# Kernel tuning notes

Hardware: AMD Instinct MI355X
Metric: run time of the kernel (lower is better)

## Reference

```python
import jax, jax.numpy as jnp
import numpy as np

CHUNK = 128
KERNEL_EPS = 1e-4
ATTN_EPS = 1e-6


def _gaussian_orthogonal_random_matrix(nb_rows, nb_cols, seed=0):
    # scaling=0: rows of stacked orthogonal blocks, scaled by chi-distributed norms
    rng = np.random.default_rng(seed)
    blocks = []
    n_full = nb_rows // nb_cols
    for _ in range(n_full):
        qm, _ = np.linalg.qr(rng.standard_normal((nb_cols, nb_cols)))
        blocks.append(qm.T)
    rem = nb_rows - n_full * nb_cols
    if rem > 0:
        qm, _ = np.linalg.qr(rng.standard_normal((nb_cols, nb_cols)))
        blocks.append(qm.T[:rem])
    mat = np.concatenate(blocks, axis=0)
    multiplier = np.linalg.norm(rng.standard_normal((nb_rows, nb_cols)), axis=1)
    return (multiplier[:, None] * mat).astype(np.float32)


def softmax_kernel(data, proj, is_query):
    # data: [b,h,n,d], proj: [m,d]
    d = data.shape[-1]
    m = proj.shape[0]
    data_normalizer = d ** -0.25
    ratio = m ** -0.5
    data_dash = jnp.einsum('bhnd,md->bhnm', data * data_normalizer, proj)
    diag_data = (data ** 2).sum(-1, keepdims=True) * 0.5 * (data_normalizer ** 2)
    if is_query:
        stab = jnp.max(data_dash, axis=-1, keepdims=True)
    else:
        stab = jnp.max(data_dash)
    return ratio * (jnp.exp(data_dash - diag_data - stab) + KERNEL_EPS)


def chunked_causal_linear_attention(qf, kf, v):
    # qf,kf: [b,h,n,m]; v: [b,h,n,e]
    b, h, n, m = qf.shape
    e = v.shape[-1]
    nc = n // CHUNK
    to_chunks = lambda t: t.reshape(b, h, nc, CHUNK, -1).transpose(2, 0, 1, 3, 4)
    qc, kc, vc = to_chunks(qf), to_chunks(kf), to_chunks(v)  # [nc,b,h,c,*]

    def step(carry, xs):
        Z, S = carry  # Z: [b,h,m], S: [b,h,m,e]
        q, k, vv = xs
        k_cum = Z[:, :, None, :] + jnp.cumsum(k, axis=2)          # [b,h,c,m]
        D_inv = 1.0 / jnp.einsum('bhcm,bhcm->bhc', q, k_cum + ATTN_EPS)
        ctx = jnp.einsum('bhcm,bhce->bhcme', k, vv)               # [b,h,c,m,e]
        ctx_cum = S[:, :, None, :, :] + jnp.cumsum(ctx, axis=2)
        out = jnp.einsum('bhcme,bhcm,bhc->bhce', ctx_cum, q, D_inv)
        return (k_cum[:, :, -1, :], ctx_cum[:, :, -1, :, :]), out

    Z0 = jnp.zeros((b, h, m), qf.dtype)
    S0 = jnp.zeros((b, h, m, e), qf.dtype)
    (Z, S), outs = jax.lax.scan(jax.checkpoint(step), (Z0, S0), (qc, kc, vc))
    out = outs.transpose(1, 2, 0, 3, 4).reshape(b, h, n, e)
    return out, Z, S


def setup_inputs() -> dict:
    key = jax.random.key(0)
    kq, kk, kv = jax.random.split(key, 3)
    B, H, N, D, M = 2, 8, 4096, 64, 256
    q = jax.random.normal(kq, (B, H, N, D), dtype=jnp.float32)
    k = jax.random.normal(kk, (B, H, N, D), dtype=jnp.float32)
    v = jax.random.normal(kv, (B, H, N, D), dtype=jnp.float32)
    projection_matrix = jnp.asarray(_gaussian_orthogonal_random_matrix(M, D))
    return {"q": q, "k": k, "v": v, "projection_matrix": projection_matrix,
            "inferrring_states": 1}


def reference(q, k, v, projection_matrix, inferrring_states):
    qf = softmax_kernel(q, projection_matrix, is_query=True)
    kf = softmax_kernel(k, projection_matrix, is_query=False)
    out, Z, S = chunked_causal_linear_attention(qf, kf, v)
    return (out, Z, S)
```

## Files before the change

kernel.cpp:

```cpp
#include <hip/hip_runtime.h>

typedef unsigned short ushort_t;
typedef __attribute__((ext_vector_type(8))) short bf16x8;
typedef __attribute__((ext_vector_type(8))) _Float16 f16x8;
typedef __attribute__((ext_vector_type(16))) float f32x16;

#define NORMC 0.35355339059327373f
#define DIAGC 0.0625f
#define RATIO 0.0625f
#define KEPS  1e-4f
#define AEPS  1e-6f
#define KAPPA (RATIO*KEPS)

__device__ __forceinline__ unsigned short f2bf(float f){
  unsigned u = __float_as_uint(f);
  unsigned r = (u + 0x7FFFu + ((u >> 16) & 1u)) >> 16;
  return (unsigned short)r;
}
__device__ __forceinline__ float bf2f(unsigned short h){
  return __uint_as_float(((unsigned)h) << 16);
}
__device__ __forceinline__ unsigned enc_f(float f){
  unsigned u = __float_as_uint(f);
  return (u & 0x80000000u) ? ~u : (u | 0x80000000u);
}
__device__ __forceinline__ float dec_f(unsigned e){
  unsigned b = (e & 0x80000000u) ? (e ^ 0x80000000u) : ~e;
  return __uint_as_float(b);
}
__device__ __forceinline__ unsigned short h2u(_Float16 h){
  union { _Float16 h; unsigned short u; } c; c.h = h; return c.u;
}
__device__ __forceinline__ unsigned pk2h(float a, float b){
  return (unsigned)h2u((_Float16)a) | ((unsigned)h2u((_Float16)b) << 16);
}
__device__ __forceinline__ unsigned cvt2(unsigned wrd, float alpha){
  float lo = bf2f((ushort_t)(wrd & 0xffffu));
  float hi = bf2f((ushort_t)(wrd >> 16));
  return (unsigned)f2bf(fmaf(alpha, lo, KAPPA)) |
         ((unsigned)f2bf(fmaf(alpha, hi, KAPPA)) << 16);
}

__global__ void k_prep(const float* __restrict__ proj, ushort_t* __restrict__ pjh,
                       unsigned* __restrict__ kmax){
  int t = threadIdx.x;
  if (t == 0) *kmax = 0u;
  for (int d = 0; d < 64; ++d){
    float val = NORMC * proj[t*64 + d];
    pjh[t*64 + d] = h2u((_Float16)val);
  }
}

__launch_bounds__(512, 4)
__global__ void k_feat(const float* __restrict__ q, const float* __restrict__ k,
                       const ushort_t* __restrict__ pjh,
                       ushort_t* __restrict__ qf, ushort_t* __restrict__ kfp,
                       unsigned* __restrict__ kmax, float* __restrict__ lmArr)
{
  extern __shared__ char sm[];
  char* Bp = sm;
  char* Xh = sm + 32768;
  char* Xl = sm + 49152;
  float* dsm  = (float*)(sm + 65536);
  float* rmx  = (float*)(sm + 66048);
  float* wred = (float*)(sm + 67072);

  int tid = threadIdx.x;
  int w   = tid >> 6;
  int wr  = w & 3;
  int wc  = w >> 2;
  int lane= tid & 63;
  int l31 = lane & 31;
  int half= lane >> 5;

  bool isQ = (blockIdx.x < 512);
  int tile = isQ ? (int)blockIdx.x : (int)blockIdx.x - 512;
  const float* src = isQ ? q : k;
  int row0 = tile * 128;

  for (int i = tid; i < 2048; i += 512){
    int m = i >> 3, c8 = i & 7;
    int rgn = ((m>>5)*4 + (c8>>1))*2 + (c8&1);
    int slot = (m & 31) ^ ((rgn & 7) << 2);
    *(uint4*)(Bp + rgn*512 + slot*16) = *(const uint4*)(pjh + m*64 + c8*8);
  }
  #pragma unroll
  for (int it = 0; it < 4; ++it){
    int g = it*512 + tid;
    int row = g >> 4, c4 = g & 15;
    float4 xv = *(const float4*)(src + (size_t)(row0+row)*64 + c4*4);
    _Float16 h0=(_Float16)xv.x, h1=(_Float16)xv.y, h2=(_Float16)xv.z, h3=(_Float16)xv.w;
    float l0 = xv.x-(float)h0, l1 = xv.y-(float)h1, l2 = xv.z-(float)h2, l3 = xv.w-(float)h3;
    int rgn = ((row>>5)*4 + (c4>>2))*2 + ((c4>>1)&1);
    int off = rgn*512 + (((row&31) ^ ((c4>>1)<<2)))*16 + (c4&1)*8;
    uint2 ph; ph.x = (unsigned)h2u(h0)|((unsigned)h2u(h1)<<16);
              ph.y = (unsigned)h2u(h2)|((unsigned)h2u(h3)<<16);
    uint2 pl; pl.x = pk2h(l0,l1); pl.y = pk2h(l2,l3);
    *(uint2*)(Xh + off) = ph;
    *(uint2*)(Xl + off) = pl;
    float ssq = xv.x*xv.x + xv.y*xv.y + xv.z*xv.z + xv.w*xv.w;
    ssq += __shfl_xor(ssq, 1); ssq += __shfl_xor(ssq, 2);
    ssq += __shfl_xor(ssq, 4); ssq += __shfl_xor(ssq, 8);
    if ((tid & 15) == 0) dsm[row] = ssq;
  }
  __syncthreads();

  f16x8 ah[4], al[4];
  #pragma unroll
  for (int ks = 0; ks < 4; ++ks){
    int rgn = (wr*4+ks)*2+half;
    int off = rgn*512 + ((l31 ^ ((2*ks+half)<<2)))*16;
    ah[ks] = *(const f16x8*)(Xh + off);
    al[ks] = *(const f16x8*)(Xl + off);
  }
  f32x16 acc[4];
  #pragma unroll
  for (int ct=0; ct<4; ++ct){
    #pragma unroll
    for (int r=0; r<16; ++r) acc[ct][r] = 0.f;
  }
  #pragma unroll
  for (int ks = 0; ks < 4; ++ks){
    #pragma unroll
    for (int ct=0; ct<4; ++ct){
      int ctg = wc*4 + ct;
      int rgn = (ctg*4+ks)*2+half;
      f16x8 bv = *(const f16x8*)(Bp + rgn*512 + ((l31 ^ ((2*ks+half)<<2)))*16);
      acc[ct] = __builtin_amdgcn_mfma_f32_32x32x16_f16(ah[ks], bv, acc[ct], 0, 0, 0);
      acc[ct] = __builtin_amdgcn_mfma_f32_32x32x16_f16(al[ks], bv, acc[ct], 0, 0, 0);
    }
  }

  float rmax[16];
  #pragma unroll
  for (int r=0; r<16; ++r){
    float mx = acc[0][r];
    #pragma unroll
    for (int ct=1; ct<4; ++ct) mx = fmaxf(mx, acc[ct][r]);
    #pragma unroll
    for (int s=1; s<32; s<<=1) mx = fmaxf(mx, __shfl_xor(mx, s));
    rmax[r] = mx;
  }
  if (isQ){
    if (l31 == 0){
      #pragma unroll
      for (int r=0; r<16; ++r)
        rmx[wc*128 + 32*wr + (r&3) + 8*(r>>2) + 4*half] = rmax[r];
    }
  } else {
    float wm = rmax[0];
    #pragma unroll
    for (int r=1; r<16; ++r) wm = fmaxf(wm, rmax[r]);
    wm = fmaxf(wm, __shfl_xor(wm, 32));
    if (lane == 0) wred[w] = wm;
  }
  __syncthreads();

  float lmb = 0.f;
  if (!isQ){
    lmb = wred[0];
    #pragma unroll
    for (int i=1;i<8;++i) lmb = fmaxf(lmb, wred[i]);
    if (tid == 0){
      lmArr[tile] = lmb;
      atomicMax(kmax, enc_f(lmb));
    }
  }
  float dgv[16], stv[16];
  #pragma unroll
  for (int r=0; r<16; ++r){
    int lrow = 32*wr + (r&3) + 8*(r>>2) + 4*half;
    dgv[r] = DIAGC * dsm[lrow];
    stv[r] = isQ ? fmaxf(rmx[lrow], rmx[128+lrow]) : lmb;
  }

  char* ob = sm;
  #pragma unroll
  for (int r=0; r<16; ++r){
    int lrow = 32*wr + (r&3) + 8*(r>>2) + 4*half;
    #pragma unroll
    for (int ct=0; ct<4; ++ct){
      int col = wc*128 + ct*32 + l31;
      float e = __expf(acc[ct][r] - dgv[r] - stv[r]);
      float val = isQ ? RATIO*(e + KEPS) : e;
      *(ushort_t*)(ob + lrow*512 + ((col*2) ^ ((lrow&15)<<4))) = f2bf(val);
    }
  }
  __syncthreads();
  ushort_t* dst = (isQ ? qf : kfp) + (size_t)row0*256;
  for (int i = tid; i < 4096; i += 512){
    int row = i >> 5, s = i & 31;
    uint4 d = *(const uint4*)(ob + row*512 + ((s*16) ^ ((row&15)<<4)));
    *(uint4*)(dst + (size_t)row*256 + ((s ^ (row&15)))*8) = d;
  }
}

__launch_bounds__(256)
__global__ void k_chunk(const ushort_t* __restrict__ kfp, const float* __restrict__ v,
                        float* __restrict__ Zl, float* __restrict__ Sl,
                        const float* __restrict__ lmArr, const unsigned* __restrict__ kmax){
  extern __shared__ char sm[];
  char* kT = sm;
  char* vT = sm + 65536;
  int tid = threadIdx.x;
  int w   = tid >> 6;
  int lane= tid & 63;
  int l31 = lane & 31;
  int half= lane >> 5;
  int bh = blockIdx.x >> 5, j = blockIdx.x & 31;
  int row0 = bh*4096 + j*128;
  int cb = bh*32 + j;

  float gmv = dec_f(*kmax);
  float alpha = RATIO * __expf(lmArr[cb] - gmv);

  {
    const ushort_t* kp = kfp + (size_t)row0*256 + tid;
    char* krow = kT + tid*256;
    int swz = (tid & 15) << 4;
    #pragma unroll 16
    for (int c=0; c<128; ++c){
      float val = fmaf(alpha, bf2f(kp[(size_t)c*256]), KAPPA);
      *(ushort_t*)(krow + ((c*2) ^ swz)) = f2bf(val);
    }
  }
  {
    int e = tid & 63; int c0 = tid >> 6;
    char* vrow = vT + e*256;
    int swz = (e & 15) << 4;
    #pragma unroll 8
    for (int u=0; u<32; ++u){
      int c = c0 + u*4;
      float vv = v[(size_t)(row0+c)*64 + e];
      *(ushort_t*)(vrow + ((c*2) ^ swz)) = f2bf(vv);
    }
  }
  __syncthreads();

  f32x16 acc[2][2];
  f32x16 accz[2];
  #pragma unroll
  for (int a=0;a<2;++a){
    #pragma unroll
    for (int b=0;b<2;++b){
      #pragma unroll
      for (int r=0;r<16;++r) acc[a][b][r]=0.f;
    }
    #pragma unroll
    for (int r=0;r<16;++r) accz[a][r]=0.f;
  }
  bf16x8 onesf;
  #pragma unroll
  for (int i=0;i<8;++i) onesf[i] = (l31==0) ? (short)0x3F80 : (short)0;

  #pragma unroll
  for (int ks=0; ks<8; ++ks){
    int koff = ks*32 + half*16;
    bf16x8 af[2], bf[2];
    #pragma unroll
    for (int mt=0; mt<2; ++mt){
      int m = (2*w + mt)*32 + l31;
      af[mt] = *(const bf16x8*)(kT + m*256 + (koff ^ ((m&15)<<4)));
    }
    #pragma unroll
    for (int et=0; et<2; ++et){
      int e = et*32 + l31;
      bf[et] = *(const bf16x8*)(vT + e*256 + (koff ^ ((e&15)<<4)));
    }
    #pragma unroll
    for (int mt=0; mt<2; ++mt){
      accz[mt] = __builtin_amdgcn_mfma_f32_32x32x16_bf16(af[mt], onesf, accz[mt], 0, 0, 0);
      #pragma unroll
      for (int et=0; et<2; ++et)
        acc[mt][et] = __builtin_amdgcn_mfma_f32_32x32x16_bf16(af[mt], bf[et], acc[mt][et], 0, 0, 0);
    }
  }

  #pragma unroll
  for (int mt=0; mt<2; ++mt){
    #pragma unroll
    for (int r=0; r<16; ++r){
      int m = (2*w + mt)*32 + (r&3) + 8*(r>>2) + 4*half;
      #pragma unroll
      for (int et=0; et<2; ++et){
        int e = et*32 + l31;
        Sl[(size_t)cb*16384 + (size_t)m*64 + e] = acc[mt][et][r];
      }
    }
  }
  if (l31 == 0){
    #pragma unroll
    for (int mt=0; mt<2; ++mt){
      #pragma unroll
      for (int r=0; r<16; ++r){
        int m = (2*w + mt)*32 + (r&3) + 8*(r>>2) + 4*half;
        Zl[(size_t)cb*256 + m] = accz[mt][r];
      }
    }
  }
}

__launch_bounds__(256)
__global__ void k_scan(float* __restrict__ Zl, const float* __restrict__ Sl,
                       ushort_t* __restrict__ S0b,
                       float* __restrict__ outZ, float* __restrict__ outS){
  int t = threadIdx.x;
  int bh = blockIdx.x / 65;
  int s  = blockIdx.x % 65;
  if (s == 64){
    size_t base = (size_t)(bh*32)*256 + t;
    float rz = 0.f;
    #pragma unroll
    for (int j0=0;j0<32;j0+=8){
      float x[8];
      #pragma unroll
      for (int u=0;u<8;++u) x[u] = Zl[base + (size_t)(j0+u)*256];
      #pragma unroll
      for (int u=0;u<8;++u){ Zl[base + (size_t)(j0+u)*256] = rz; rz += x[u]; }
    }
    outZ[(size_t)bh*256 + t] = rz;
  } else {
    size_t base = (size_t)(bh*32)*16384 + (size_t)s*256 + t;
    float rs = 0.f;
    #pragma unroll
    for (int j0=0;j0<32;j0+=8){
      float x[8];
      #pragma unroll
      for (int u=0;u<8;++u) x[u] = Sl[base + (size_t)(j0+u)*16384];
      #pragma unroll
      for (int u=0;u<8;++u){
        S0b[(size_t)(bh*32 + j0+u)*16384 + (size_t)s*256 + t] = f2bf(rs);
        rs += x[u];
      }
    }
    outS[(size_t)bh*16384 + (size_t)s*256 + t] = rs;
  }
}

__launch_bounds__(256)
__global__ void k_out(const ushort_t* __restrict__ qf, const ushort_t* __restrict__ kfp,
                      const float* __restrict__ v, const ushort_t* __restrict__ S0b,
                      const float* __restrict__ Zp, float* __restrict__ outO,
                      const float* __restrict__ lmArr, const unsigned* __restrict__ kmax){
  extern __shared__ char smc[];
  char* Ab  = smc;
  char* qtb = smc + 32768;
  char* ktb = smc + 49152;
  char* s0t = smc + 65536;
  float* z0  = (float*)(smc + 73728);
  float* qzl = (float*)(smc + 74752);
  float* rsum= (float*)(smc + 75264);

  int tid = threadIdx.x;
  int w   = tid >> 6;
  int lane= tid & 63;
  int l31 = lane & 31;
  int half= lane >> 5;
  int arow= 32*w + l31;
  int bh = blockIdx.x >> 5, j = blockIdx.x & 31;
  int row0 = bh*4096 + j*128;
  size_t qbase = (size_t)row0*256;
  int pb = bh*32 + j;

  float gmv = dec_f(*kmax);
  float alpha = RATIO * __expf(lmArr[pb] - gmv);

  z0[tid] = Zp[(size_t)pb*256 + tid] + AEPS;
  float qzp = 0.f;

  f32x16 acc[4];
  f32x16 acc2[2];
  #pragma unroll
  for (int ct=0;ct<4;++ct){
    #pragma unroll
    for (int r=0;r<16;++r) acc[ct][r] = 0.f;
  }
  #pragma unroll
  for (int et=0;et<2;++et){
    #pragma unroll
    for (int r=0;r<16;++r) acc2[et][r] = 0.f;
  }

  for (int m0=0;m0<256;m0+=64){
    __syncthreads();
    #pragma unroll
    for (int u=0;u<4;++u){
      int ci = tid*4+u; int rr = ci>>3, c8 = ci&7;
      int sw = (c8*16) ^ ((rr&7)<<4);
      uint4 rq = *(const uint4*)(qf + qbase + (size_t)rr*256 + m0 + c8*8);
      *(uint4*)(qtb + rr*128 + sw) = rq;
      float4 za = *(const float4*)&z0[m0 + c8*8];
      float4 zb = *(const float4*)&z0[m0 + c8*8 + 4];
      qzp += bf2f((ushort_t)(rq.x&0xffffu))*za.x + bf2f((ushort_t)(rq.x>>16))*za.y
           + bf2f((ushort_t)(rq.y&0xffffu))*za.z + bf2f((ushort_t)(rq.y>>16))*za.w
           + bf2f((ushort_t)(rq.z&0xffffu))*zb.x + bf2f((ushort_t)(rq.z>>16))*zb.y
           + bf2f((ushort_t)(rq.w&0xffffu))*zb.z + bf2f((ushort_t)(rq.w>>16))*zb.w;
      uint4 rk = *(const uint4*)(kfp + qbase + (size_t)rr*256 + m0 + c8*8);
      uint4 ck; ck.x = cvt2(rk.x, alpha); ck.y = cvt2(rk.y, alpha);
                ck.z = cvt2(rk.z, alpha); ck.w = cvt2(rk.w, alpha);
      *(uint4*)(ktb + rr*128 + sw) = ck;
    }
    #pragma unroll
    for (int u=0;u<2;++u){
      int idx = u*256 + tid; int mm = idx>>3, c8 = idx&7;
      uint4 sv = *(const uint4*)(S0b + (size_t)pb*16384 + (size_t)(m0+mm)*64 + c8*8);
      unsigned wds[4] = {sv.x, sv.y, sv.z, sv.w};
      #pragma unroll
      for (int jj=0;jj<4;++jj){
        int e0 = c8*8 + jj*2;
        int e1 = e0 + 1;
        int sw0 = ((e0&7) ^ ((e0>>3)&7)) << 4;
        int sw1 = ((e1&7) ^ ((e1>>3)&7)) << 4;
        *(ushort_t*)(s0t + e0*128 + ((mm*2) ^ sw0)) = (ushort_t)(wds[jj] & 0xffffu);
        *(ushort_t*)(s0t + e1*128 + ((mm*2) ^ sw1)) = (ushort_t)(wds[jj] >> 16);
      }
    }
    __syncthreads();
    #pragma unroll
    for (int ks=0;ks<4;++ks){
      bf16x8 af = *(const bf16x8*)(qtb + arow*128 + ((ks*32 + half*16) ^ ((arow&7)<<4)));
      #pragma unroll
      for (int et=0;et<2;++et){
        int er = et*32 + l31;
        int sw = ((er&7) ^ ((er>>3)&7)) << 4;
        bf16x8 bS = *(const bf16x8*)(s0t + er*128 + ((ks*32 + half*16) ^ sw));
        acc2[et] = __builtin_amdgcn_mfma_f32_32x32x16_bf16(af, bS, acc2[et], 0, 0, 0);
      }
      #pragma unroll
      for (int ct=0;ct<4;++ct){
        if (ct <= w){
          int br = ct*32 + l31;
          bf16x8 bfv = *(const bf16x8*)(ktb + br*128 + ((ks*32 + half*16) ^ ((br&7)<<4)));
          acc[ct] = __builtin_amdgcn_mfma_f32_32x32x16_bf16(af, bfv, acc[ct], 0, 0, 0);
        }
      }
    }
  }

  qzp += __shfl_xor(qzp, 1);
  if ((tid & 1) == 0) qzl[tid>>1] = qzp;

  float p[16];
  #pragma unroll
  for (int r=0;r<16;++r) p[r]=0.f;
  #pragma unroll
  for (int ct=0;ct<4;++ct){
    #pragma unroll
    for (int r=0;r<16;++r){
      int grow = 32*w + (r&3) + 8*(r>>2) + 4*half;
      int col  = ct*32 + l31;
      float m = (col <= grow) ? acc[ct][r] : 0.f;
      p[r] += m;
      *(ushort_t*)(Ab + grow*256 + ((col*2) ^ ((grow&15)<<4))) = f2bf(m);
    }
  }
  #pragma unroll
  for (int s=1;s<32;s<<=1){
    #pragma unroll
    for (int r=0;r<16;++r) p[r] += __shfl_xor(p[r], s);
  }
  if (l31 == 0){
    #pragma unroll
    for (int r=0;r<16;++r) rsum[32*w + (r&3) + 8*(r>>2) + 4*half] = p[r];
  }
  __syncthreads();

  for (int kt=0; kt<2; ++kt){
    #pragma unroll
    for (int u=0;u<4;++u){
      int idx = tid*4+u; int rr = idx>>4, c4 = idx&15;
      float4 vv = *(const float4*)&v[(size_t)(row0 + kt*64 + rr)*64 + c4*4];
      float vals[4] = {vv.x, vv.y, vv.z, vv.w};
      #pragma unroll
      for (int jj=0;jj<4;++jj){
        int e = c4*4 + jj;
        int sw = ((e&7) ^ ((e>>3)&7)) << 4;
        *(ushort_t*)(s0t + e*128 + ((rr*2) ^ sw)) = f2bf(vals[jj]);
      }
    }
    __syncthreads();
    #pragma unroll
    for (int ks=0;ks<4;++ks){
      if (kt*64 + ks*16 <= 32*w + 31){
        bf16x8 af = *(const bf16x8*)(Ab + arow*256 + ((kt*128 + ks*32 + half*16) ^ ((arow&15)<<4)));
        #pragma unroll
        for (int et=0;et<2;++et){
          int er = et*32 + l31;
          int sw = ((er&7) ^ ((er>>3)&7)) << 4;
          bf16x8 bfv = *(const bf16x8*)(s0t + er*128 + ((ks*32 + half*16) ^ sw));
          acc2[et] = __builtin_amdgcn_mfma_f32_32x32x16_bf16(af, bfv, acc2[et], 0, 0, 0);
        }
      }
    }
    __syncthreads();
  }

  if (tid < 128) rsum[tid] = 1.0f / (rsum[tid] + qzl[tid]);
  __syncthreads();
  float dvv[16];
  #pragma unroll
  for (int r=0;r<16;++r) dvv[r] = rsum[32*w + (r&3) + 8*(r>>2) + 4*half];
  #pragma unroll
  for (int et=0;et<2;++et){
    #pragma unroll
    for (int r=0;r<16;++r){
      int qrow = 32*w + (r&3) + 8*(r>>2) + 4*half;
      int e = et*32 + l31;
      outO[(size_t)(row0+qrow)*64 + e] = acc2[et][r] * dvv[r];
    }
  }
}

extern "C" void kernel_launch(void* const* d_in, const int* in_sizes, int n_in,
                              void* d_out, int out_size, void* d_ws, size_t ws_size,
                              hipStream_t stream){
  (void)in_sizes; (void)n_in; (void)out_size; (void)ws_size;
  const float* q    = (const float*)d_in[0];
  const float* k    = (const float*)d_in[1];
  const float* v    = (const float*)d_in[2];
  const float* proj = (const float*)d_in[3];

  char* ws = (char*)d_ws;
  unsigned* kmax = (unsigned*)ws;
  float*    lmA  = (float*)(ws + 256);
  ushort_t* pjh  = (ushort_t*)(ws + 4096);
  ushort_t* qf   = (ushort_t*)(ws + 65792);
  ushort_t* kfp  = (ushort_t*)(ws + 65792 + 33554432);
  float*    Zl   = (float*)(ws + 65792 + 67108864);
  float*    Sl   = (float*)(ws + 65792 + 67108864 + 524288);
  ushort_t* S0b  = (ushort_t*)(ws + 65792 + 67108864 + 524288 + 33554432);

  float* outO = (float*)d_out;
  float* outZ = outO + (size_t)2*8*4096*64;
  float* outS = outZ + 2*8*256;

  hipFuncSetAttribute((const void*)k_feat,  hipFuncAttributeMaxDynamicSharedMemorySize, 67104);
  hipFuncSetAttribute((const void*)k_chunk, hipFuncAttributeMaxDynamicSharedMemorySize, 81920);
  hipFuncSetAttribute((const void*)k_out,   hipFuncAttributeMaxDynamicSharedMemorySize, 75776);

  k_prep <<<1,      256, 0, stream>>>(proj, pjh, kmax);
  k_feat <<<1024,   512, 67104, stream>>>(q, k, pjh, qf, kfp, kmax, lmA);
  k_chunk<<<512,    256, 81920, stream>>>(kfp, v, Zl, Sl, lmA, kmax);
  k_scan <<<16*65,  256, 0, stream>>>(Zl, Sl, S0b, outZ, outS);
  k_out  <<<512,    256, 75776, stream>>>(qf, kfp, v, S0b, Zl, outO, lmA, kmax);
}
```

Before: 93.91 us.

## Fuse key features into chunk kernel and query features into output kernel

Merges the feature-map kernel into the per-chunk state kernel for keys and into the output kernel for queries, so the bf16 query features are never written to or read back from global memory. The global-max rescaling (alpha and the epsilon term) is moved out of the chunk kernel and applied in the scan, using a new per-chunk v column-sum buffer to fold the KAPPA contribution back in. This removes one launch and a large intermediate round trip. In exchange, shared memory per block grows considerably (about 145 KB and 124 KB) with 512-thread blocks, which limits occupancy, and the rescaling now happens in fp32 after a bf16 matmul on unscaled features, which shifts where rounding occurs.

```diff
diff --git a/kernel.cpp b/kernel.cpp
--- a/kernel.cpp
+++ b/kernel.cpp
@@ -51,19 +51,22 @@
   }
 }
 
-__launch_bounds__(512, 4)
-__global__ void k_feat(const float* __restrict__ q, const float* __restrict__ k,
-                       const ushort_t* __restrict__ pjh,
-                       ushort_t* __restrict__ qf, ushort_t* __restrict__ kfp,
-                       unsigned* __restrict__ kmax, float* __restrict__ lmArr)
+__launch_bounds__(512, 2)
+__global__ void k_chunkF(const float* __restrict__ kk, const float* __restrict__ v,
+                         const ushort_t* __restrict__ pjh,
+                         ushort_t* __restrict__ kfp, float* __restrict__ Zl,
+                         float* __restrict__ Sl, float* __restrict__ vsb,
+                         unsigned* __restrict__ kmax, float* __restrict__ lmArr)
 {
   extern __shared__ char sm[];
   char* Bp = sm;
   char* Xh = sm + 32768;
   char* Xl = sm + 49152;
-  float* dsm  = (float*)(sm + 65536);
-  float* rmx  = (float*)(sm + 66048);
-  float* wred = (float*)(sm + 67072);
+  char* ob = sm;
+  char* kT = sm + 65536;
+  char* vT = sm + 131072;
+  float* dsm  = (float*)(sm + 147456);
+  float* wred = (float*)(sm + 147968);
 
   int tid = threadIdx.x;
   int w   = tid >> 6;
@@ -72,11 +75,9 @@
   int lane= tid & 63;
   int l31 = lane & 31;
   int half= lane >> 5;
-
-  bool isQ = (blockIdx.x < 512);
-  int tile = isQ ? (int)blockIdx.x : (int)blockIdx.x - 512;
-  const float* src = isQ ? q : k;
-  int row0 = tile * 128;
+  int cb  = (int)blockIdx.x;
+  int bh  = cb >> 5, j = cb & 31;
+  int row0 = bh*4096 + j*128;
 
   for (int i = tid; i < 2048; i += 512){
     int m = i >> 3, c8 = i & 7;
@@ -88,7 +89,7 @@
   for (int it = 0; it < 4; ++it){
     int g = it*512 + tid;
     int row = g >> 4, c4 = g & 15;
-    float4 xv = *(const float4*)(src + (size_t)(row0+row)*64 + c4*4);
+    float4 xv = *(const float4*)(kk + (size_t)(row0+row)*64 + c4*4);
     _Float16 h0=(_Float16)xv.x, h1=(_Float16)xv.y, h2=(_Float16)xv.z, h3=(_Float16)xv.w;
     float l0 = xv.x-(float)h0, l1 = xv.y-(float)h1, l2 = xv.z-(float)h2, l3 = xv.w-(float)h3;
     int rgn = ((row>>5)*4 + (c4>>2))*2 + ((c4>>1)&1);
@@ -103,6 +104,15 @@
     ssq += __shfl_xor(ssq, 4); ssq += __shfl_xor(ssq, 8);
     if ((tid & 15) == 0) dsm[row] = ssq;
   }
+  {
+    int e = tid & 63, c0 = tid >> 6;
+    int swz = (e & 15) << 4;
+    #pragma unroll
+    for (int u=0; u<16; ++u){
+      int c = c0 + u*8;
+      *(ushort_t*)(vT + e*256 + ((c*2) ^ swz)) = f2bf(v[(size_t)(row0+c)*64 + e]);
+    }
+  }
   __syncthreads();
 
   f16x8 ah[4], al[4];
@@ -131,179 +141,118 @@
     }
   }
 
-  float rmax[16];
-  #pragma unroll
-  for (int r=0; r<16; ++r){
-    float mx = acc[0][r];
-    #pragma unroll
-    for (int ct=1; ct<4; ++ct) mx = fmaxf(mx, acc[ct][r]);
-    #pragma unroll
-    for (int s=1; s<32; s<<=1) mx = fmaxf(mx, __shfl_xor(mx, s));
-    rmax[r] = mx;
-  }
-  if (isQ){
-    if (l31 == 0){
-      #pragma unroll
-      for (int r=0; r<16; ++r)
-        rmx[wc*128 + 32*wr + (r&3) + 8*(r>>2) + 4*half] = rmax[r];
-    }
-  } else {
-    float wm = rmax[0];
-    #pragma unroll
-    for (int r=1; r<16; ++r) wm = fmaxf(wm, rmax[r]);
+  {
+    float wm = acc[0][0];
+    #pragma unroll
+    for (int ct=0; ct<4; ++ct){
+      #pragma unroll
+      for (int r=0; r<16; ++r) wm = fmaxf(wm, acc[ct][r]);
+    }
+    #pragma unroll
+    for (int s=1; s<32; s<<=1) wm = fmaxf(wm, __shfl_xor(wm, s));
     wm = fmaxf(wm, __shfl_xor(wm, 32));
     if (lane == 0) wred[w] = wm;
   }
   __syncthreads();
-
-  float lmb = 0.f;
-  if (!isQ){
-    lmb = wred[0];
-    #pragma unroll
-    for (int i=1;i<8;++i) lmb = fmaxf(lmb, wred[i]);
-    if (tid == 0){
-      lmArr[tile] = lmb;
-      atomicMax(kmax, enc_f(lmb));
-    }
-  }
-  float dgv[16], stv[16];
-  #pragma unroll
-  for (int r=0; r<16; ++r){
-    int lrow = 32*wr + (r&3) + 8*(r>>2) + 4*half;
-    dgv[r] = DIAGC * dsm[lrow];
-    stv[r] = isQ ? fmaxf(rmx[lrow], rmx[128+lrow]) : lmb;
-  }
-
-  char* ob = sm;
-  #pragma unroll
-  for (int r=0; r<16; ++r){
-    int lrow = 32*wr + (r&3) + 8*(r>>2) + 4*half;
-    #pragma unroll
-    for (int ct=0; ct<4; ++ct){
-      int col = wc*128 + ct*32 + l31;
-      float e = __expf(acc[ct][r] - dgv[r] - stv[r]);
-      float val = isQ ? RATIO*(e + KEPS) : e;
-      *(ushort_t*)(ob + lrow*512 + ((col*2) ^ ((lrow&15)<<4))) = f2bf(val);
-    }
-  }
-  __syncthreads();
-  ushort_t* dst = (isQ ? qf : kfp) + (size_t)row0*256;
-  for (int i = tid; i < 4096; i += 512){
-    int row = i >> 5, s = i & 31;
-    uint4 d = *(const uint4*)(ob + row*512 + ((s*16) ^ ((row&15)<<4)));
-    *(uint4*)(dst + (size_t)row*256 + ((s ^ (row&15)))*8) = d;
-  }
-}
-
-__launch_bounds__(256)
-__global__ void k_chunk(const ushort_t* __restrict__ kfp, const float* __restrict__ v,
-                        float* __restrict__ Zl, float* __restrict__ Sl,
-                        const float* __restrict__ lmArr, const unsigned* __restrict__ kmax){
-  extern __shared__ char sm[];
-  char* kT = sm;
-  char* vT = sm + 65536;
-  int tid = threadIdx.x;
-  int w   = tid >> 6;
-  int lane= tid & 63;
-  int l31 = lane & 31;
-  int half= lane >> 5;
-  int bh = blockIdx.x >> 5, j = blockIdx.x & 31;
-  int row0 = bh*4096 + j*128;
-  int cb = bh*32 + j;
-
-  float gmv = dec_f(*kmax);
-  float alpha = RATIO * __expf(lmArr[cb] - gmv);
-
-  {
-    const ushort_t* kp = kfp + (size_t)row0*256 + tid;
-    char* krow = kT + tid*256;
-    int swz = (tid & 15) << 4;
-    #pragma unroll 16
-    for (int c=0; c<128; ++c){
-      float val = fmaf(alpha, bf2f(kp[(size_t)c*256]), KAPPA);
-      *(ushort_t*)(krow + ((c*2) ^ swz)) = f2bf(val);
-    }
-  }
-  {
-    int e = tid & 63; int c0 = tid >> 6;
-    char* vrow = vT + e*256;
-    int swz = (e & 15) << 4;
-    #pragma unroll 8
-    for (int u=0; u<32; ++u){
-      int c = c0 + u*4;
-      float vv = v[(size_t)(row0+c)*64 + e];
-      *(ushort_t*)(vrow + ((c*2) ^ swz)) = f2bf(vv);
-    }
-  }
-  __syncthreads();
-
-  f32x16 acc[2][2];
-  f32x16 accz[2];
-  #pragma unroll
-  for (int a=0;a<2;++a){
-    #pragma unroll
-    for (int b=0;b<2;++b){
-      #pragma unroll
-      for (int r=0;r<16;++r) acc[a][b][r]=0.f;
-    }
-    #pragma unroll
-    for (int r=0;r<16;++r) accz[a][r]=0.f;
-  }
-  bf16x8 onesf;
-  #pragma unroll
-  for (int i=0;i<8;++i) onesf[i] = (l31==0) ? (short)0x3F80 : (short)0;
-
+  float lmb = wred[0];
+  #pragma unroll
+  for (int i=1;i<8;++i) lmb = fmaxf(lmb, wred[i]);
+  if (tid == 0){
+    lmArr[cb] = lmb;
+    atomicMax(kmax, enc_f(lmb));
+  }
+  float dgv[16];
+  #pragma unroll
+  for (int r=0; r<16; ++r)
+    dgv[r] = DIAGC * dsm[32*wr + (r&3) + 8*(r>>2) + 4*half];
+
+  #pragma unroll
+  for (int ct=0; ct<4; ++ct){
+    int m = wc*128 + ct*32 + l31;
+    int swm = (m & 15) << 4;
+    #pragma unroll
+    for (int g=0; g<4; ++g){
+      unsigned pk0=0, pk1=0;
+      #pragma unroll
+      for (int rr=0; rr<4; ++rr){
+        int r = g*4 + rr;
+        int c = 32*wr + rr + 8*g + 4*half;
+        float e = __expf(acc[ct][r] - dgv[r] - lmb);
+        unsigned b = f2bf(e);
+        if (rr < 2) pk0 |= b << (16*rr); else pk1 |= b << (16*(rr-2));
+        *(ushort_t*)(ob + c*512 + ((m*2) ^ ((c&15)<<4))) = (ushort_t)b;
+      }
+      int c0 = 32*wr + 8*g + 4*half;
+      *(uint2*)(kT + m*256 + ((c0*2) ^ swm)) = make_uint2(pk0, pk1);
+    }
+  }
+  __syncthreads();
+
+  f32x16 acc2[2], accz, avs[2];
+  #pragma unroll
+  for (int et=0;et<2;++et){
+    #pragma unroll
+    for (int r=0;r<16;++r){ acc2[et][r]=0.f; avs[et][r]=0.f; }
+  }
+  #pragma unroll
+  for (int r=0;r<16;++r) accz[r]=0.f;
+  bf16x8 onesB, onesA;
+  #pragma unroll
+  for (int i=0;i<8;++i){
+    onesB[i] = (l31==0) ? (short)0x3F80 : (short)0;
+    onesA[i] = (short)0x3F80;
+  }
+  int mrow = 32*w + l31;
+  int swm2 = (mrow & 15) << 4;
   #pragma unroll
   for (int ks=0; ks<8; ++ks){
     int koff = ks*32 + half*16;
-    bf16x8 af[2], bf[2];
-    #pragma unroll
-    for (int mt=0; mt<2; ++mt){
-      int m = (2*w + mt)*32 + l31;
-      af[mt] = *(const bf16x8*)(kT + m*256 + (koff ^ ((m&15)<<4)));
-    }
-    #pragma unroll
-    for (int et=0; et<2; ++et){
-      int e = et*32 + l31;
-      bf[et] = *(const bf16x8*)(vT + e*256 + (koff ^ ((e&15)<<4)));
-    }
-    #pragma unroll
-    for (int mt=0; mt<2; ++mt){
-      accz[mt] = __builtin_amdgcn_mfma_f32_32x32x16_bf16(af[mt], onesf, accz[mt], 0, 0, 0);
-      #pragma unroll
-      for (int et=0; et<2; ++et)
-        acc[mt][et] = __builtin_amdgcn_mfma_f32_32x32x16_bf16(af[mt], bf[et], acc[mt][et], 0, 0, 0);
-    }
-  }
-
-  #pragma unroll
-  for (int mt=0; mt<2; ++mt){
+    bf16x8 af = *(const bf16x8*)(kT + mrow*256 + (koff ^ swm2));
+    bf16x8 b0 = *(const bf16x8*)(vT + (l31)*256      + (koff ^ ((l31&15)<<4)));
+    bf16x8 b1 = *(const bf16x8*)(vT + (32+l31)*256   + (koff ^ (((32+l31)&15)<<4)));
+    acc2[0] = __builtin_amdgcn_mfma_f32_32x32x16_bf16(af, b0, acc2[0], 0, 0, 0);
+    acc2[1] = __builtin_amdgcn_mfma_f32_32x32x16_bf16(af, b1, acc2[1], 0, 0, 0);
+    accz    = __builtin_amdgcn_mfma_f32_32x32x16_bf16(af, onesB, accz, 0, 0, 0);
+    if (w == 0){
+      avs[0] = __builtin_amdgcn_mfma_f32_32x32x16_bf16(onesA, b0, avs[0], 0, 0, 0);
+      avs[1] = __builtin_amdgcn_mfma_f32_32x32x16_bf16(onesA, b1, avs[1], 0, 0, 0);
+    }
+  }
+  #pragma unroll
+  for (int r=0; r<16; ++r){
+    int m = 32*w + (r&3) + 8*(r>>2) + 4*half;
+    #pragma unroll
+    for (int et=0; et<2; ++et)
+      Sl[(size_t)cb*16384 + (size_t)m*64 + et*32 + l31] = acc2[et][r];
+  }
+  if (l31 == 0){
     #pragma unroll
     for (int r=0; r<16; ++r){
-      int m = (2*w + mt)*32 + (r&3) + 8*(r>>2) + 4*half;
-      #pragma unroll
-      for (int et=0; et<2; ++et){
-        int e = et*32 + l31;
-        Sl[(size_t)cb*16384 + (size_t)m*64 + e] = acc[mt][et][r];
-      }
-    }
-  }
-  if (l31 == 0){
-    #pragma unroll
-    for (int mt=0; mt<2; ++mt){
-      #pragma unroll
-      for (int r=0; r<16; ++r){
-        int m = (2*w + mt)*32 + (r&3) + 8*(r>>2) + 4*half;
-        Zl[(size_t)cb*256 + m] = accz[mt][r];
-      }
+      int m = 32*w + (r&3) + 8*(r>>2) + 4*half;
+      Zl[(size_t)cb*256 + m] = accz[r];
+    }
+  }
+  if (w == 0 && half == 0){
+    vsb[(size_t)cb*64 + l31]      = avs[0][0];
+    vsb[(size_t)cb*64 + 32 + l31] = avs[1][0];
+  }
+  {
+    ushort_t* dst = kfp + (size_t)row0*256;
+    for (int i = tid; i < 4096; i += 512){
+      int row = i >> 5, s = i & 31;
+      uint4 d = *(const uint4*)(ob + row*512 + ((s*16) ^ ((row&15)<<4)));
+      *(uint4*)(dst + (size_t)row*256 + ((s ^ (row&15)))*8) = d;
     }
   }
 }
 
 __launch_bounds__(256)
 __global__ void k_scan(float* __restrict__ Zl, const float* __restrict__ Sl,
+                       const float* __restrict__ vsb, const float* __restrict__ lmArr,
+                       const unsigned* __restrict__ kmax,
                        ushort_t* __restrict__ S0b,
                        float* __restrict__ outZ, float* __restrict__ outS){
+  float gm = dec_f(*kmax);
   int t = threadIdx.x;
   int bh = blockIdx.x / 65;
   int s  = blockIdx.x % 65;
@@ -314,19 +263,28 @@
     for (int j0=0;j0<32;j0+=8){
       float x[8];
       #pragma unroll
-      for (int u=0;u<8;++u) x[u] = Zl[base + (size_t)(j0+u)*256];
+      for (int u=0;u<8;++u){
+        int cbx = bh*32 + j0 + u;
+        float a = RATIO * __expf(lmArr[cbx] - gm);
+        x[u] = fmaf(a, Zl[base + (size_t)(j0+u)*256], KAPPA*128.f);
+      }
       #pragma unroll
       for (int u=0;u<8;++u){ Zl[base + (size_t)(j0+u)*256] = rz; rz += x[u]; }
     }
     outZ[(size_t)bh*256 + t] = rz;
   } else {
+    int e = t & 63;
     size_t base = (size_t)(bh*32)*16384 + (size_t)s*256 + t;
     float rs = 0.f;
     #pragma unroll
     for (int j0=0;j0<32;j0+=8){
       float x[8];
       #pragma unroll
-      for (int u=0;u<8;++u) x[u] = Sl[base + (size_t)(j0+u)*16384];
+      for (int u=0;u<8;++u){
+        int cbx = bh*32 + j0 + u;
+        float a = RATIO * __expf(lmArr[cbx] - gm);
+        x[u] = fmaf(a, Sl[base + (size_t)(j0+u)*16384], KAPPA * vsb[(size_t)cbx*64 + e]);
+      }
       #pragma unroll
       for (int u=0;u<8;++u){
         S0b[(size_t)(bh*32 + j0+u)*16384 + (size_t)s*256 + t] = f2bf(rs);
@@ -337,78 +295,179 @@
   }
 }
 
-__launch_bounds__(256)
-__global__ void k_out(const ushort_t* __restrict__ qf, const ushort_t* __restrict__ kfp,
-                      const float* __restrict__ v, const ushort_t* __restrict__ S0b,
-                      const float* __restrict__ Zp, float* __restrict__ outO,
-                      const float* __restrict__ lmArr, const unsigned* __restrict__ kmax){
-  extern __shared__ char smc[];
-  char* Ab  = smc;
-  char* qtb = smc + 32768;
-  char* ktb = smc + 49152;
-  char* s0t = smc + 65536;
-  float* z0  = (float*)(smc + 73728);
-  float* qzl = (float*)(smc + 74752);
-  float* rsum= (float*)(smc + 75264);
+__launch_bounds__(512, 2)
+__global__ void k_outF(const float* __restrict__ q, const ushort_t* __restrict__ pjh,
+                       const ushort_t* __restrict__ kfp, const float* __restrict__ v,
+                       const ushort_t* __restrict__ S0b, const float* __restrict__ Zp,
+                       const float* __restrict__ lmArr, const unsigned* __restrict__ kmax,
+                       float* __restrict__ outO)
+{
+  extern __shared__ char sm[];
+  char* Bp  = sm;
+  char* Ab  = sm;
+  char* qfb = sm + 32768;
+  char* Xh  = sm + 32768;
+  char* Xl  = sm + 49152;
+  char* ktb = sm + 98304;
+  char* s0t = sm + 114688;
+  char* vTb = sm + 98304;
+  float* dsm = (float*)(sm + 122880);
+  float* rmx = (float*)(sm + 123392);
+  float* qzc = (float*)(sm + 124416);
+  float* rsc = (float*)(sm + 125440);
+  float* rsf = (float*)(sm + 126464);
 
   int tid = threadIdx.x;
   int w   = tid >> 6;
+  int wr  = w & 3;
+  int wc  = w >> 2;
   int lane= tid & 63;
   int l31 = lane & 31;
   int half= lane >> 5;
-  int arow= 32*w + l31;
-  int bh = blockIdx.x >> 5, j = blockIdx.x & 31;
+  int pb  = (int)blockIdx.x;
+  int bh  = pb >> 5, j = pb & 31;
   int row0 = bh*4096 + j*128;
   size_t qbase = (size_t)row0*256;
-  int pb = bh*32 + j;
 
   float gmv = dec_f(*kmax);
   float alpha = RATIO * __expf(lmArr[pb] - gmv);
 
-  z0[tid] = Zp[(size_t)pb*256 + tid] + AEPS;
-  float qzp = 0.f;
-
+  for (int i = tid; i < 2048; i += 512){
+    int m = i >> 3, c8 = i & 7;
+    int rgn = ((m>>5)*4 + (c8>>1))*2 + (c8&1);
+    int slot = (m & 31) ^ ((rgn & 7) << 2);
+    *(uint4*)(Bp + rgn*512 + slot*16) = *(const uint4*)(pjh + m*64 + c8*8);
+  }
+  #pragma unroll
+  for (int it = 0; it < 4; ++it){
+    int g = it*512 + tid;
+    int row = g >> 4, c4 = g & 15;
+    float4 xv = *(const float4*)(q + (size_t)(row0+row)*64 + c4*4);
+    _Float16 h0=(_Float16)xv.x, h1=(_Float16)xv.y, h2=(_Float16)xv.z, h3=(_Float16)xv.w;
+    float l0 = xv.x-(float)h0, l1 = xv.y-(float)h1, l2 = xv.z-(float)h2, l3 = xv.w-(float)h3;
+    int rgn = ((row>>5)*4 + (c4>>2))*2 + ((c4>>1)&1);
+    int off = rgn*512 + (((row&31) ^ ((c4>>1)<<2)))*16 + (c4&1)*8;
+    uint2 ph; ph.x = (unsigned)h2u(h0)|((unsigned)h2u(h1)<<16);
+              ph.y = (unsigned)h2u(h2)|((unsigned)h2u(h3)<<16);
+    uint2 pl; pl.x = pk2h(l0,l1); pl.y = pk2h(l2,l3);
+    *(uint2*)(Xh + off) = ph;
+    *(uint2*)(Xl + off) = pl;
+    float ssq = xv.x*xv.x + xv.y*xv.y + xv.z*xv.z + xv.w*xv.w;
+    ssq += __shfl_xor(ssq, 1); ssq += __shfl_xor(ssq, 2);
+    ssq += __shfl_xor(ssq, 4); ssq += __shfl_xor(ssq, 8);
+    if ((tid & 15) == 0) dsm[row] = ssq;
+  }
+  __syncthreads();
+
+  f16x8 ah[4], al[4];
+  #pragma unroll
+  for (int ks = 0; ks < 4; ++ks){
+    int rgn = (wr*4+ks)*2+half;
+    int off = rgn*512 + ((l31 ^ ((2*ks+half)<<2)))*16;
+    ah[ks] = *(const f16x8*)(Xh + off);
+    al[ks] = *(const f16x8*)(Xl + off);
+  }
   f32x16 acc[4];
-  f32x16 acc2[2];
-  #pragma unroll
-  for (int ct=0;ct<4;++ct){
-    #pragma unroll
-    for (int r=0;r<16;++r) acc[ct][r] = 0.f;
-  }
-  #pragma unroll
-  for (int et=0;et<2;++et){
-    #pragma unroll
-    for (int r=0;r<16;++r) acc2[et][r] = 0.f;
-  }
-
-  for (int m0=0;m0<256;m0+=64){
+  #pragma unroll
+  for (int ct=0; ct<4; ++ct){
+    #pragma unroll
+    for (int r=0; r<16; ++r) acc[ct][r] = 0.f;
+  }
+  #pragma unroll
+  for (int ks = 0; ks < 4; ++ks){
+    #pragma unroll
+    for (int ct=0; ct<4; ++ct){
+      int ctg = wc*4 + ct;
+      int rgn = (ctg*4+ks)*2+half;
+      f16x8 bv = *(const f16x8*)(Bp + rgn*512 + ((l31 ^ ((2*ks+half)<<2)))*16);
+      acc[ct] = __builtin_amdgcn_mfma_f32_32x32x16_f16(ah[ks], bv, acc[ct], 0, 0, 0);
+      acc[ct] = __builtin_amdgcn_mfma_f32_32x32x16_f16(al[ks], bv, acc[ct], 0, 0, 0);
+    }
+  }
+  {
+    float rmax[16];
+    #pragma unroll
+    for (int r=0; r<16; ++r){
+      float mx = acc[0][r];
+      #pragma unroll
+      for (int ct=1; ct<4; ++ct) mx = fmaxf(mx, acc[ct][r]);
+      #pragma unroll
+      for (int s=1; s<32; s<<=1) mx = fmaxf(mx, __shfl_xor(mx, s));
+      rmax[r] = mx;
+    }
+    if (l31 == 0){
+      #pragma unroll
+      for (int r=0; r<16; ++r)
+        rmx[wc*128 + 32*wr + (r&3) + 8*(r>>2) + 4*half] = rmax[r];
+    }
+  }
+  __syncthreads();
+
+  float qzp[16];
+  #pragma unroll
+  for (int r=0;r<16;++r) qzp[r] = 0.f;
+  {
+    float dgv[16], stv[16];
+    #pragma unroll
+    for (int r=0; r<16; ++r){
+      int lrow = 32*wr + (r&3) + 8*(r>>2) + 4*half;
+      dgv[r] = DIAGC * dsm[lrow];
+      stv[r] = fmaxf(rmx[lrow], rmx[128+lrow]);
+    }
+    #pragma unroll
+    for (int ct=0; ct<4; ++ct){
+      int m = wc*128 + ct*32 + l31;
+      float z0v = Zp[(size_t)pb*256 + m] + AEPS;
+      #pragma unroll
+      for (int r=0; r<16; ++r){
+        int c = 32*wr + (r&3) + 8*(r>>2) + 4*half;
+        float e = __expf(acc[ct][r] - dgv[r] - stv[r]);
+        unsigned b = f2bf(RATIO*(e + KEPS));
+        *(ushort_t*)(qfb + c*512 + ((m*2) ^ ((c&15)<<4))) = (ushort_t)b;
+        qzp[r] += bf2f((ushort_t)b) * z0v;
+      }
+    }
+    #pragma unroll
+    for (int s=1; s<32; s<<=1){
+      #pragma unroll
+      for (int r=0;r<16;++r) qzp[r] += __shfl_xor(qzp[r], s);
+    }
+    if (l31 == 0){
+      #pragma unroll
+      for (int r=0;r<16;++r)
+        qzc[wc*128 + 32*wr + (r&3) + 8*(r>>2) + 4*half] = qzp[r];
+    }
+  }
+
+  f32x16 accA[2], acc2;
+  #pragma unroll
+  for (int ct2=0;ct2<2;++ct2){
+    #pragma unroll
+    for (int r=0;r<16;++r) accA[ct2][r] = 0.f;
+  }
+  #pragma unroll
+  for (int r=0;r<16;++r) acc2[r] = 0.f;
+
+  int arow = 32*wr + l31;
+  for (int mt=0; mt<4; ++mt){
+    int m0 = mt*64;
     __syncthreads();
     #pragma unroll
-    for (int u=0;u<4;++u){
-      int ci = tid*4+u; int rr = ci>>3, c8 = ci&7;
+    for (int u=0;u<2;++u){
+      int ci = tid*2+u; int rr = ci>>3, c8 = ci&7;
       int sw = (c8*16) ^ ((rr&7)<<4);
-      uint4 rq = *(const uint4*)(qf + qbase + (size_t)rr*256 + m0 + c8*8);
-      *(uint4*)(qtb + rr*128 + sw) = rq;
-      float4 za = *(const float4*)&z0[m0 + c8*8];
-      float4 zb = *(const float4*)&z0[m0 + c8*8 + 4];
-      qzp += bf2f((ushort_t)(rq.x&0xffffu))*za.x + bf2f((ushort_t)(rq.x>>16))*za.y
-           + bf2f((ushort_t)(rq.y&0xffffu))*za.z + bf2f((ushort_t)(rq.y>>16))*za.w
-           + bf2f((ushort_t)(rq.z&0xffffu))*zb.x + bf2f((ushort_t)(rq.z>>16))*zb.y
-           + bf2f((ushort_t)(rq.w&0xffffu))*zb.z + bf2f((ushort_t)(rq.w>>16))*zb.w;
       uint4 rk = *(const uint4*)(kfp + qbase + (size_t)rr*256 + m0 + c8*8);
       uint4 ck; ck.x = cvt2(rk.x, alpha); ck.y = cvt2(rk.y, alpha);
                 ck.z = cvt2(rk.z, alpha); ck.w = cvt2(rk.w, alpha);
       *(uint4*)(ktb + rr*128 + sw) = ck;
     }
-    #pragma unroll
-    for (int u=0;u<2;++u){
-      int idx = u*256 + tid; int mm = idx>>3, c8 = idx&7;
+    {
+      int mm = tid >> 3, c8 = tid & 7;
       uint4 sv = *(const uint4*)(S0b + (size_t)pb*16384 + (size_t)(m0+mm)*64 + c8*8);
       unsigned wds[4] = {sv.x, sv.y, sv.z, sv.w};
       #pragma unroll
       for (int jj=0;jj<4;++jj){
-        int e0 = c8*8 + jj*2;
-        int e1 = e0 + 1;
+        int e0 = c8*8 + jj*2, e1 = e0 + 1;
         int sw0 = ((e0&7) ^ ((e0>>3)&7)) << 4;
         int sw1 = ((e1&7) ^ ((e1>>3)&7)) << 4;
         *(ushort_t*)(s0t + e0*128 + ((mm*2) ^ sw0)) = (ushort_t)(wds[jj] & 0xffffu);
@@ -418,96 +477,85 @@
     __syncthreads();
     #pragma unroll
     for (int ks=0;ks<4;++ks){
-      bf16x8 af = *(const bf16x8*)(qtb + arow*128 + ((ks*32 + half*16) ^ ((arow&7)<<4)));
-      #pragma unroll
-      for (int et=0;et<2;++et){
-        int er = et*32 + l31;
+      bf16x8 af = *(const bf16x8*)(qfb + arow*512 + ((m0*2 + ks*32 + half*16) ^ ((arow&15)<<4)));
+      {
+        int er = wc*32 + l31;
         int sw = ((er&7) ^ ((er>>3)&7)) << 4;
         bf16x8 bS = *(const bf16x8*)(s0t + er*128 + ((ks*32 + half*16) ^ sw));
-        acc2[et] = __builtin_amdgcn_mfma_f32_32x32x16_bf16(af, bS, acc2[et], 0, 0, 0);
-      }
-      #pragma unroll
-      for (int ct=0;ct<4;++ct){
-        if (ct <= w){
-          int br = ct*32 + l31;
+        acc2 = __builtin_amdgcn_mfma_f32_32x32x16_bf16(af, bS, acc2, 0, 0, 0);
+      }
+      #pragma unroll
+      for (int ct2=0;ct2<2;++ct2){
+        int c = wc*2 + ct2;
+        if (c <= wr){
+          int br = c*32 + l31;
           bf16x8 bfv = *(const bf16x8*)(ktb + br*128 + ((ks*32 + half*16) ^ ((br&7)<<4)));
-          acc[ct] = __builtin_amdgcn_mfma_f32_32x32x16_bf16(af, bfv, acc[ct], 0, 0, 0);
+          accA[ct2] = __builtin_amdgcn_mfma_f32_32x32x16_bf16(af, bfv, accA[ct2], 0, 0, 0);
         }
       }
     }
   }
 
-  qzp += __shfl_xor(qzp, 1);
-  if ((tid & 1) == 0) qzl[tid>>1] = qzp;
-
-  float p[16];
-  #pragma unroll
-  for (int r=0;r<16;++r) p[r]=0.f;
-  #pragma unroll
-  for (int ct=0;ct<4;++ct){
-    #pragma unroll
-    for (int r=0;r<16;++r){
-      int grow = 32*w + (r&3) + 8*(r>>2) + 4*half;
-      int col  = ct*32 + l31;
-      float m = (col <= grow) ? acc[ct][r] : 0.f;
-      p[r] += m;
-      *(ushort_t*)(Ab + grow*256 + ((col*2) ^ ((grow&15)<<4))) = f2bf(m);
-    }
-  }
-  #pragma unroll
-  for (int s=1;s<32;s<<=1){
-    #pragma unroll
-    for (int r=0;r<16;++r) p[r] += __shfl_xor(p[r], s);
-  }
-  if (l31 == 0){
-    #pragma unroll
-    for (int r=0;r<16;++r) rsum[32*w + (r&3) + 8*(r>>2) + 4*half] = p[r];
-  }
-  __syncthreads();
-
-  for (int kt=0; kt<2; ++kt){
-    #pragma unroll
-    for (int u=0;u<4;++u){
-      int idx = tid*4+u; int rr = idx>>4, c4 = idx&15;
-      float4 vv = *(const float4*)&v[(size_t)(row0 + kt*64 + rr)*64 + c4*4];
-      float vals[4] = {vv.x, vv.y, vv.z, vv.w};
-      #pragma unroll
-      for (int jj=0;jj<4;++jj){
-        int e = c4*4 + jj;
-        int sw = ((e&7) ^ ((e>>3)&7)) << 4;
-        *(ushort_t*)(s0t + e*128 + ((rr*2) ^ sw)) = f2bf(vals[jj]);
-      }
-    }
-    __syncthreads();
-    #pragma unroll
-    for (int ks=0;ks<4;++ks){
-      if (kt*64 + ks*16 <= 32*w + 31){
-        bf16x8 af = *(const bf16x8*)(Ab + arow*256 + ((kt*128 + ks*32 + half*16) ^ ((arow&15)<<4)));
+  {
+    float p[16];
+    #pragma unroll
+    for (int r=0;r<16;++r) p[r]=0.f;
+    #pragma unroll
+    for (int ct2=0;ct2<2;++ct2){
+      int c = wc*2 + ct2;
+      if (c <= wr){
         #pragma unroll
-        for (int et=0;et<2;++et){
-          int er = et*32 + l31;
-          int sw = ((er&7) ^ ((er>>3)&7)) << 4;
-          bf16x8 bfv = *(const bf16x8*)(s0t + er*128 + ((ks*32 + half*16) ^ sw));
-          acc2[et] = __builtin_amdgcn_mfma_f32_32x32x16_bf16(af, bfv, acc2[et], 0, 0, 0);
+        for (int r=0;r<16;++r){
+          int grow = 32*wr + (r&3) + 8*(r>>2) + 4*half;
+          int col  = c*32 + l31;
+          float mval = (col <= grow) ? accA[ct2][r] : 0.f;
+          p[r] += mval;
+          *(ushort_t*)(Ab + grow*256 + ((col*2) ^ ((grow&15)<<4))) = f2bf(mval);
         }
       }
     }
-    __syncthreads();
-  }
-
-  if (tid < 128) rsum[tid] = 1.0f / (rsum[tid] + qzl[tid]);
-  __syncthreads();
-  float dvv[16];
-  #pragma unroll
-  for (int r=0;r<16;++r) dvv[r] = rsum[32*w + (r&3) + 8*(r>>2) + 4*half];
-  #pragma unroll
-  for (int et=0;et<2;++et){
-    #pragma unroll
-    for (int r=0;r<16;++r){
-      int qrow = 32*w + (r&3) + 8*(r>>2) + 4*half;
-      int e = et*32 + l31;
-      outO[(size_t)(row0+qrow)*64 + e] = acc2[et][r] * dvv[r];
-    }
+    #pragma unroll
+    for (int s=1;s<32;s<<=1){
+      #pragma unroll
+      for (int r=0;r<16;++r) p[r] += __shfl_xor(p[r], s);
+    }
+    if (l31 == 0){
+      #pragma unroll
+      for (int r=0;r<16;++r)
+        rsc[wc*128 + 32*wr + (r&3) + 8*(r>>2) + 4*half] = p[r];
+    }
+  }
+  __syncthreads();
+
+  {
+    int e = tid & 63, c0 = tid >> 6;
+    int swz = (e & 15) << 4;
+    #pragma unroll
+    for (int u=0; u<16; ++u){
+      int c = c0 + u*8;
+      *(ushort_t*)(vTb + e*256 + ((c*2) ^ swz)) = f2bf(v[(size_t)(row0+c)*64 + e]);
+    }
+  }
+  __syncthreads();
+
+  #pragma unroll
+  for (int ks=0; ks<8; ++ks){
+    if (ks <= 2*wr + 1){
+      bf16x8 af = *(const bf16x8*)(Ab + arow*256 + ((ks*32 + half*16) ^ ((arow&15)<<4)));
+      int er = wc*32 + l31;
+      bf16x8 bfv = *(const bf16x8*)(vTb + er*256 + ((ks*32 + half*16) ^ ((er&15)<<4)));
+      acc2 = __builtin_amdgcn_mfma_f32_32x32x16_bf16(af, bfv, acc2, 0, 0, 0);
+    }
+  }
+  __syncthreads();
+  if (tid < 128)
+    rsf[tid] = 1.0f / (rsc[tid] + rsc[128+tid] + qzc[tid] + qzc[128+tid]);
+  __syncthreads();
+  #pragma unroll
+  for (int r=0;r<16;++r){
+    int grow = 32*wr + (r&3) + 8*(r>>2) + 4*half;
+    int e = wc*32 + l31;
+    outO[(size_t)(row0+grow)*64 + e] = acc2[r] * rsf[grow];
   }
 }
 
@@ -524,23 +572,21 @@
   unsigned* kmax = (unsigned*)ws;
   float*    lmA  = (float*)(ws + 256);
   ushort_t* pjh  = (ushort_t*)(ws + 4096);
-  ushort_t* qf   = (ushort_t*)(ws + 65792);
-  ushort_t* kfp  = (ushort_t*)(ws + 65792 + 33554432);
-  float*    Zl   = (float*)(ws + 65792 + 67108864);
-  float*    Sl   = (float*)(ws + 65792 + 67108864 + 524288);
-  ushort_t* S0b  = (ushort_t*)(ws + 65792 + 67108864 + 524288 + 33554432);
+  ushort_t* kfp  = (ushort_t*)(ws + 65792);
+  float*    Zl   = (float*)(ws + 65792 + 33554432);
+  float*    Sl   = (float*)(ws + 65792 + 33554432 + 524288);
+  ushort_t* S0b  = (ushort_t*)(ws + 65792 + 67633152);
+  float*    vsb  = (float*)(ws + 65792 + 67633152 + 16777216);
 
   float* outO = (float*)d_out;
   float* outZ = outO + (size_t)2*8*4096*64;
   float* outS = outZ + 2*8*256;
 
-  hipFuncSetAttribute((const void*)k_feat,  hipFuncAttributeMaxDynamicSharedMemorySize, 67104);
-  hipFuncSetAttribute((const void*)k_chunk, hipFuncAttributeMaxDynamicSharedMemorySize, 81920);
-  hipFuncSetAttribute((const void*)k_out,   hipFuncAttributeMaxDynamicSharedMemorySize, 75776);
-
-  k_prep <<<1,      256, 0, stream>>>(proj, pjh, kmax);
-  k_feat <<<1024,   512, 67104, stream>>>(q, k, pjh, qf, kfp, kmax, lmA);
-  k_chunk<<<512,    256, 81920, stream>>>(kfp, v, Zl, Sl, lmA, kmax);
-  k_scan <<<16*65,  256, 0, stream>>>(Zl, Sl, S0b, outZ, outS);
-  k_out  <<<512,    256, 75776, stream>>>(qf, kfp, v, S0b, Zl, outO, lmA, kmax);
-}
+  hipFuncSetAttribute((const void*)k_chunkF, hipFuncAttributeMaxDynamicSharedMemorySize, 148480);
+  hipFuncSetAttribute((const void*)k_outF,   hipFuncAttributeMaxDynamicSharedMemorySize, 126976);
+
+  k_prep  <<<1,     256, 0, stream>>>(proj, pjh, kmax);
+  k_chunkF<<<512,   512, 148480, stream>>>(k, v, pjh, kfp, Zl, Sl, vsb, kmax, lmA);
+  k_scan  <<<16*65, 256, 0, stream>>>(Zl, Sl, vsb, lmA, kmax, S0b, outZ, outS);
+  k_outF  <<<512,   512, 126976, stream>>>(q, pjh, kfp, v, S0b, Zl, lmA, kmax, outO);
+}
```

Result: slower. 98.24 us (+4.6%).
